# Kernel tuning notes

Hardware: AMD Instinct MI355X
Metric: run time of the kernel (lower is better)

Reference implementation:

```python
import jax, jax.numpy as jnp
import numpy as np


def setup_inputs() -> dict:
    key = jax.random.key(0)
    k1, k2, k3 = jax.random.split(key, 3)
    B, C, H, W = 4, 256, 96, 128
    F = 9
    return {
        "input1": jax.random.normal(k1, (B, C, H, W), dtype=jnp.float32),
        "input2": jax.random.normal(k2, (B, C, H, W), dtype=jnp.float32),
        "weights": jax.random.normal(k3, (C, F, F), dtype=jnp.float32),
        "filter_size": 9,
        "dilation": 2,
        "num_groups": 4,
    }


def _weighted_corr(input1, input2, weights, filter_size, dilation, num_groups):
    B, C, H, W = input1.shape
    F = filter_size
    G = num_groups
    Cg = C // G
    r = F // 2
    pad = r * dilation
    # zero-pad input2 spatially so out-of-bounds displacements contribute 0
    p2 = jnp.pad(input2, ((0, 0), (0, 0), (pad, pad), (pad, pad)))
    in1g = input1.reshape(B, G, Cg, H, W)
    outs = []  # one [B, G, H, W] map per window offset (dy, dx)
    for dy in range(F):
        for dx in range(F):
            shifted = p2[:, :, dy * dilation:dy * dilation + H,
                         dx * dilation:dx * dilation + W].reshape(B, G, Cg, H, W)
            wg = weights[:, dy, dx].reshape(G, Cg)
            outs.append(jnp.einsum('bgchw,bgchw,gc->bghw', in1g, shifted, wg))
    out = jnp.stack(outs, axis=2)  # [B, G, F*F, H, W]
    return out.reshape(B, G * F * F, H, W)


def reference(input1, input2, weights, filter_size, dilation, num_groups):
    return _weighted_corr(input1, input2, weights, filter_size, dilation, num_groups)
```

## Files before the change

### kernel.cpp

```cpp
#include <hip/hip_runtime.h>

#define B_   4
#define C_   256
#define H_   96
#define W_   128
#define F_   9
#define G_   4
#define CG   64
#define NC8  8
#define NO   81
#define HW_  (H_ * W_)

#define NDY   3
#define TROWS 8
#define TCOLS 80
#define PTE   (TROWS * TCOLS)
#define PNK   3

typedef _Float16 half2v __attribute__((ext_vector_type(2)));
typedef unsigned u32x4 __attribute__((ext_vector_type(4)));

__device__ __forceinline__ half2v u2h(unsigned u) {
    half2v h; __builtin_memcpy(&h, &u, 4); return h;
}
__device__ __forceinline__ unsigned h2u(half2v h) {
    unsigned u; __builtin_memcpy(&u, &h, 4); return u;
}
__device__ __forceinline__ half2v pkrtz(float a, float b) {
    auto r = __builtin_amdgcn_cvt_pkrtz(a, b);
    half2v h; __builtin_memcpy(&h, &r, 4); return h;
}
__device__ __forceinline__ unsigned pkrtz_u(float a, float b) {
    auto r = __builtin_amdgcn_cvt_pkrtz(a, b);
    unsigned u; __builtin_memcpy(&u, &r, 4); return u;
}

#if __has_builtin(__builtin_amdgcn_fdot2)
#define FDOT2(a, b, c) __builtin_amdgcn_fdot2((a), (b), (c), false)
#else
__device__ __forceinline__ float fdot2_fb(half2v a, half2v b, float c) {
    return c + (float)a[0] * (float)b[0] + (float)a[1] * (float)b[1];
}
#define FDOT2(a, b, c) fdot2_fb((a), (b), (c))
#endif

__global__ void pack_weights_kernel(const float* __restrict__ w,
                                    u32x4* __restrict__ wp) {
    int i = blockIdx.x * blockDim.x + threadIdx.x;
    if (i >= G_ * NC8 * NO) return;
    int o  = i % NO;
    int c8 = (i / NO) % NC8;
    int g  = i / (NO * NC8);
    const float* base = w + (size_t)(g * CG + 8 * c8) * NO + o;
    u32x4 r;
    r.x = pkrtz_u(base[0 * NO], base[1 * NO]);
    r.y = pkrtz_u(base[2 * NO], base[3 * NO]);
    r.z = pkrtz_u(base[4 * NO], base[5 * NO]);
    r.w = pkrtz_u(base[6 * NO], base[7 * NO]);
    wp[i] = r;
}

template <bool PACKED>
__global__ __launch_bounds__(256)
void wcorr_kernel(const float* __restrict__ in1, const float* __restrict__ in2,
                  const u32x4* __restrict__ wp, const float* __restrict__ wraw,
                  float* __restrict__ out) {
    __shared__ u32x4 tile[2][PTE];

    int bid  = blockIdx.x;
    int xcd  = bid & 7;
    int slot = bid >> 3;
    int pair = xcd + 8 * (slot / 144);
    int rem  = slot % 144;
    int pass = rem / 48;
    int sub  = rem % 48;
    int hblk = sub >> 1;
    int half = sub & 1;
    int b = pair >> 2, g = pair & 3;
    int h0 = hblk * 4;
    int w0 = half * 64;

    int t = threadIdx.x;
    int r = t >> 6;
    int x = t & 63;

    const float* in1g = in1 + (size_t)(b * C_ + g * CG) * HW_;
    const float* in2g = in2 + (size_t)(b * C_ + g * CG) * HW_;

    const int gr0 = h0 - 8 + 6 * pass;
    const int gc0 = w0 - 8;
    int po[PNK]; unsigned msk[PNK];
#pragma unroll
    for (int k = 0; k < PNK; ++k) {
        int pidx = k * 256 + t;
        int row  = pidx / TCOLS;
        int col  = pidx - row * TCOLS;
        int gr = gr0 + row, gc = gc0 + col;
        bool inb = (pidx < PTE) && gr >= 0 && gr < H_ && gc >= 0 && gc < W_;
        int off = gr * W_ + gc;
        off = off < 0 ? 0 : (off > HW_ - 1 ? HW_ - 1 : off);
        po[k]  = off;
        float m = inb ? 1.f : 0.f;
        msk[k] = pkrtz_u(m, m);
    }

    float acc[NDY * F_];
#pragma unroll
    for (int o = 0; o < NDY * F_; ++o) acc[o] = 0.f;

    float sv[PNK][8];

    auto LOADS = [&](int c8n) {
        const float* chb = in2g + (size_t)(8 * c8n) * HW_;
#pragma unroll
        for (int k = 0; k < PNK; ++k) {
            const float* q = chb + po[k];
#pragma unroll
            for (int j = 0; j < 8; ++j) sv[k][j] = q[(size_t)j * HW_];
        }
    };
    auto WRITE = [&](u32x4* dst) {
#pragma unroll
        for (int k = 0; k < PNK; ++k) {
            if (k < PNK - 1 || t < PTE - (PNK - 1) * 256) {
                half2v m = u2h(msk[k]);
                u32x4 e;
                e.x = h2u(u2h(pkrtz_u(sv[k][0], sv[k][1])) * m);
                e.y = h2u(u2h(pkrtz_u(sv[k][2], sv[k][3])) * m);
                e.z = h2u(u2h(pkrtz_u(sv[k][4], sv[k][5])) * m);
                e.w = h2u(u2h(pkrtz_u(sv[k][6], sv[k][7])) * m);
                dst[k * 256 + t] = e;
            }
        }
    };

    LOADS(0);
    WRITE(tile[0]);
    LOADS(1);

    const int in1off = (h0 + r) * W_ + (w0 + x);
    float a[8];
#pragma unroll
    for (int j = 0; j < 8; ++j) a[j] = in1g[in1off + (size_t)j * HW_];

    for (int c8 = 0; c8 < NC8; ++c8) {
        __syncthreads();

        if (c8 + 1 < NC8) WRITE(tile[(c8 + 1) & 1]);
        if (c8 + 2 < NC8) LOADS(c8 + 2);

        half2v ha0 = pkrtz(a[0], a[1]), ha1 = pkrtz(a[2], a[3]);
        half2v ha2 = pkrtz(a[4], a[5]), ha3 = pkrtz(a[6], a[7]);
        if (c8 + 1 < NC8) {
            const float* pp = in1g + (size_t)(8 * (c8 + 1)) * HW_ + in1off;
#pragma unroll
            for (int j = 0; j < 8; ++j) a[j] = pp[(size_t)j * HW_];
        }

        const u32x4* lt = tile[c8 & 1];
        const u32x4* wrow = PACKED ? (wp + ((size_t)g * NC8 + c8) * NO + pass * NDY * F_) : nullptr;
        const float* wr = wraw + (size_t)(g * CG + 8 * c8) * NO + pass * NDY * F_;

#pragma unroll
        for (int dyp = 0; dyp < NDY; ++dyp) {
            const u32x4* rowp = lt + (r + 2 * dyp) * TCOLS + x;
#pragma unroll
            for (int dx = 0; dx < F_; ++dx) {
                const int oo = dyp * F_ + dx;
                u32x4 uv = rowp[2 * dx];
                half2v w0h, w1h, w2h, w3h;
                if (PACKED) {
                    u32x4 wv = wrow[oo];
                    w0h = u2h(wv.x); w1h = u2h(wv.y);
                    w2h = u2h(wv.z); w3h = u2h(wv.w);
                } else {
                    w0h = pkrtz(wr[oo + 0 * NO], wr[oo + 1 * NO]);
                    w1h = pkrtz(wr[oo + 2 * NO], wr[oo + 3 * NO]);
                    w2h = pkrtz(wr[oo + 4 * NO], wr[oo + 5 * NO]);
                    w3h = pkrtz(wr[oo + 6 * NO], wr[oo + 7 * NO]);
                }
                float s = acc[oo];
                s = FDOT2(w0h * ha0, u2h(uv.x), s);
                s = FDOT2(w1h * ha1, u2h(uv.y), s);
                s = FDOT2(w2h * ha2, u2h(uv.z), s);
                s = FDOT2(w3h * ha3, u2h(uv.w), s);
                acc[oo] = s;
            }
        }
    }

    size_t obase = (((size_t)pair * NO + pass * NDY * F_) * H_ + (h0 + r)) * W_ + (w0 + x);
#pragma unroll
    for (int oo = 0; oo < NDY * F_; ++oo)
        out[obase + (size_t)oo * HW_] = acc[oo];
}

extern "C" void kernel_launch(void* const* d_in, const int* in_sizes, int n_in,
                              void* d_out, int out_size, void* d_ws, size_t ws_size,
                              hipStream_t stream) {
    const float* in1  = (const float*)d_in[0];
    const float* in2  = (const float*)d_in[1];
    const float* wraw = (const float*)d_in[2];
    float* out = (float*)d_out;

    const size_t wp_bytes = (size_t)G_ * NC8 * NO * 16;
    const int nblocks = 16 * 144;

    if (ws_size >= wp_bytes) {
        u32x4* wp = (u32x4*)d_ws;
        int n = G_ * NC8 * NO;
        pack_weights_kernel<<<(n + 255) / 256, 256, 0, stream>>>(wraw, wp);
        wcorr_kernel<true><<<nblocks, 256, 0, stream>>>(in1, in2, wp, wraw, out);
    } else {
        wcorr_kernel<false><<<nblocks, 256, 0, stream>>>(in1, in2, nullptr, wraw, out);
    }
}
```

Measured before the change: 74.60 us.

## Tile per single dy row with two outputs per thread sharing LDS reads

Each block now covers one dy and four full-width output rows, and each thread computes two output columns two apart. Because dilation is 2, both columns can share 10 LDS reads where 18 were needed before. The LDS tile is split by column parity with an XOR swizzle to avoid bank conflicts. in1 loads are now done per iteration with no prefetch, so their global latency is exposed, and the accumulator/grid shape changes (3456 blocks, 18 accumulators per thread).

```diff
diff --git a/kernel.cpp b/kernel.cpp
--- a/kernel.cpp
+++ b/kernel.cpp
@@ -11,10 +11,10 @@
 #define NO   81
 #define HW_  (H_ * W_)
 
-#define NDY   3
-#define TROWS 8
-#define TCOLS 80
-#define PTE   (TROWS * TCOLS)
+#define OROWS 4
+#define TCOLS 144
+#define PCOLS 72
+#define NENT  (OROWS * 2 * PCOLS)
 #define PNK   3
 
 typedef _Float16 half2v __attribute__((ext_vector_type(2)));
@@ -43,6 +43,10 @@
 }
 #define FDOT2(a, b, c) fdot2_fb((a), (b), (c))
 #endif
+
+__device__ __forceinline__ int swz(int col2) {
+    return col2 ^ ((col2 >> 3) & 7);
+}
 
 __global__ void pack_weights_kernel(const float* __restrict__ w,
                                     u32x4* __restrict__ wp) {
@@ -65,48 +69,54 @@
 void wcorr_kernel(const float* __restrict__ in1, const float* __restrict__ in2,
                   const u32x4* __restrict__ wp, const float* __restrict__ wraw,
                   float* __restrict__ out) {
-    __shared__ u32x4 tile[2][PTE];
-
-    int bid  = blockIdx.x;
-    int xcd  = bid & 7;
-    int slot = bid >> 3;
-    int pair = xcd + 8 * (slot / 144);
-    int rem  = slot % 144;
-    int pass = rem / 48;
-    int sub  = rem % 48;
-    int hblk = sub >> 1;
-    int half = sub & 1;
+    __shared__ u32x4 tile[2][NENT];
+
+    int bid   = blockIdx.x;
+    int xcd   = bid & 7;
+    int slot  = bid >> 3;
+    int tuple = slot / 9;
+    int dy    = slot - tuple * 9;
+    int T     = tuple * 8 + xcd;
+    int pair  = T & 15;
+    int hblk  = T >> 4;
     int b = pair >> 2, g = pair & 3;
-    int h0 = hblk * 4;
-    int w0 = half * 64;
-
-    int t = threadIdx.x;
-    int r = t >> 6;
-    int x = t & 63;
+    int h0 = hblk * OROWS;
+
+    int t   = threadIdx.x;
+    int row = t >> 6;
+    int i   = t & 63;
+    int j   = i >> 1;
+    int p   = i & 1;
+    const int c0 = 4 * j + p;
 
     const float* in1g = in1 + (size_t)(b * C_ + g * CG) * HW_;
     const float* in2g = in2 + (size_t)(b * C_ + g * CG) * HW_;
 
-    const int gr0 = h0 - 8 + 6 * pass;
-    const int gc0 = w0 - 8;
-    int po[PNK]; unsigned msk[PNK];
+    const int gr0 = h0 + 2 * dy - 8;
+    int po[PNK]; unsigned msk[PNK]; int lix[PNK];
 #pragma unroll
     for (int k = 0; k < PNK; ++k) {
         int pidx = k * 256 + t;
-        int row  = pidx / TCOLS;
-        int col  = pidx - row * TCOLS;
-        int gr = gr0 + row, gc = gc0 + col;
-        bool inb = (pidx < PTE) && gr >= 0 && gr < H_ && gc >= 0 && gc < W_;
+        int srow = pidx / TCOLS;
+        int col  = pidx - srow * TCOLS;
+        int gr = gr0 + srow, gc = col - 8;
+        bool inb = (pidx < NENT) && gr >= 0 && gr < H_ && gc >= 0 && gc < W_;
         int off = gr * W_ + gc;
         off = off < 0 ? 0 : (off > HW_ - 1 ? HW_ - 1 : off);
         po[k]  = off;
         float m = inb ? 1.f : 0.f;
         msk[k] = pkrtz_u(m, m);
-    }
-
-    float acc[NDY * F_];
-#pragma unroll
-    for (int o = 0; o < NDY * F_; ++o) acc[o] = 0.f;
+        lix[k] = (srow * 2 + (col & 1)) * PCOLS + swz(col >> 1);
+    }
+
+    int widx[10];
+#pragma unroll
+    for (int m = 0; m < 10; ++m)
+        widx[m] = (row * 2 + p) * PCOLS + swz(2 * j + m);
+
+    float acc0[F_], acc1[F_];
+#pragma unroll
+    for (int dx = 0; dx < F_; ++dx) { acc0[dx] = 0.f; acc1[dx] = 0.f; }
 
     float sv[PNK][8];
 
@@ -114,22 +124,24 @@
         const float* chb = in2g + (size_t)(8 * c8n) * HW_;
 #pragma unroll
         for (int k = 0; k < PNK; ++k) {
-            const float* q = chb + po[k];
-#pragma unroll
-            for (int j = 0; j < 8; ++j) sv[k][j] = q[(size_t)j * HW_];
+            if (k < PNK - 1 || t < NENT - (PNK - 1) * 256) {
+                const float* q = chb + po[k];
+#pragma unroll
+                for (int c = 0; c < 8; ++c) sv[k][c] = q[(size_t)c * HW_];
+            }
         }
     };
     auto WRITE = [&](u32x4* dst) {
 #pragma unroll
         for (int k = 0; k < PNK; ++k) {
-            if (k < PNK - 1 || t < PTE - (PNK - 1) * 256) {
+            if (k < PNK - 1 || t < NENT - (PNK - 1) * 256) {
                 half2v m = u2h(msk[k]);
                 u32x4 e;
                 e.x = h2u(u2h(pkrtz_u(sv[k][0], sv[k][1])) * m);
                 e.y = h2u(u2h(pkrtz_u(sv[k][2], sv[k][3])) * m);
                 e.z = h2u(u2h(pkrtz_u(sv[k][4], sv[k][5])) * m);
                 e.w = h2u(u2h(pkrtz_u(sv[k][6], sv[k][7])) * m);
-                dst[k * 256 + t] = e;
+                dst[lix[k]] = e;
             }
         }
     };
@@ -138,10 +150,7 @@
     WRITE(tile[0]);
     LOADS(1);
 
-    const int in1off = (h0 + r) * W_ + (w0 + x);
-    float a[8];
-#pragma unroll
-    for (int j = 0; j < 8; ++j) a[j] = in1g[in1off + (size_t)j * HW_];
+    const int in1off = (h0 + row) * W_ + c0;
 
     for (int c8 = 0; c8 < NC8; ++c8) {
         __syncthreads();
@@ -149,50 +158,72 @@
         if (c8 + 1 < NC8) WRITE(tile[(c8 + 1) & 1]);
         if (c8 + 2 < NC8) LOADS(c8 + 2);
 
-        half2v ha0 = pkrtz(a[0], a[1]), ha1 = pkrtz(a[2], a[3]);
-        half2v ha2 = pkrtz(a[4], a[5]), ha3 = pkrtz(a[6], a[7]);
-        if (c8 + 1 < NC8) {
-            const float* pp = in1g + (size_t)(8 * (c8 + 1)) * HW_ + in1off;
-#pragma unroll
-            for (int j = 0; j < 8; ++j) a[j] = pp[(size_t)j * HW_];
+        const float* ib = in1g + (size_t)(8 * c8) * HW_ + in1off;
+        half2v ha0, ha1, ha2, ha3, hb0, hb1, hb2, hb3;
+        {
+            float x0 = ib[0], x1 = ib[HW_], x2 = ib[2 * HW_], x3 = ib[3 * HW_];
+            float x4 = ib[4 * HW_], x5 = ib[5 * HW_], x6 = ib[6 * HW_], x7 = ib[7 * HW_];
+            ha0 = pkrtz(x0, x1); ha1 = pkrtz(x2, x3);
+            ha2 = pkrtz(x4, x5); ha3 = pkrtz(x6, x7);
+            float y0 = ib[2], y1 = ib[HW_ + 2], y2 = ib[2 * HW_ + 2], y3 = ib[3 * HW_ + 2];
+            float y4 = ib[4 * HW_ + 2], y5 = ib[5 * HW_ + 2], y6 = ib[6 * HW_ + 2], y7 = ib[7 * HW_ + 2];
+            hb0 = pkrtz(y0, y1); hb1 = pkrtz(y2, y3);
+            hb2 = pkrtz(y4, y5); hb3 = pkrtz(y6, y7);
         }
 
         const u32x4* lt = tile[c8 & 1];
-        const u32x4* wrow = PACKED ? (wp + ((size_t)g * NC8 + c8) * NO + pass * NDY * F_) : nullptr;
-        const float* wr = wraw + (size_t)(g * CG + 8 * c8) * NO + pass * NDY * F_;
-
-#pragma unroll
-        for (int dyp = 0; dyp < NDY; ++dyp) {
-            const u32x4* rowp = lt + (r + 2 * dyp) * TCOLS + x;
-#pragma unroll
-            for (int dx = 0; dx < F_; ++dx) {
-                const int oo = dyp * F_ + dx;
-                u32x4 uv = rowp[2 * dx];
+        const u32x4* wrow = PACKED ? (wp + ((size_t)g * NC8 + c8) * NO + dy * F_) : nullptr;
+        const float* wr = wraw + (size_t)(g * CG + 8 * c8) * NO + dy * F_;
+
+#pragma unroll
+        for (int m = 0; m < 10; ++m) {
+            u32x4 uv = lt[widx[m]];
+            if (m <= 8) {
                 half2v w0h, w1h, w2h, w3h;
                 if (PACKED) {
-                    u32x4 wv = wrow[oo];
-                    w0h = u2h(wv.x); w1h = u2h(wv.y);
-                    w2h = u2h(wv.z); w3h = u2h(wv.w);
+                    u32x4 wv = wrow[m];
+                    w0h = u2h(wv.x); w1h = u2h(wv.y); w2h = u2h(wv.z); w3h = u2h(wv.w);
                 } else {
-                    w0h = pkrtz(wr[oo + 0 * NO], wr[oo + 1 * NO]);
-                    w1h = pkrtz(wr[oo + 2 * NO], wr[oo + 3 * NO]);
-                    w2h = pkrtz(wr[oo + 4 * NO], wr[oo + 5 * NO]);
-                    w3h = pkrtz(wr[oo + 6 * NO], wr[oo + 7 * NO]);
+                    w0h = pkrtz(wr[m + 0 * NO], wr[m + 1 * NO]);
+                    w1h = pkrtz(wr[m + 2 * NO], wr[m + 3 * NO]);
+                    w2h = pkrtz(wr[m + 4 * NO], wr[m + 5 * NO]);
+                    w3h = pkrtz(wr[m + 6 * NO], wr[m + 7 * NO]);
                 }
-                float s = acc[oo];
+                float s = acc0[m];
                 s = FDOT2(w0h * ha0, u2h(uv.x), s);
                 s = FDOT2(w1h * ha1, u2h(uv.y), s);
                 s = FDOT2(w2h * ha2, u2h(uv.z), s);
                 s = FDOT2(w3h * ha3, u2h(uv.w), s);
-                acc[oo] = s;
-            }
-        }
-    }
-
-    size_t obase = (((size_t)pair * NO + pass * NDY * F_) * H_ + (h0 + r)) * W_ + (w0 + x);
-#pragma unroll
-    for (int oo = 0; oo < NDY * F_; ++oo)
-        out[obase + (size_t)oo * HW_] = acc[oo];
+                acc0[m] = s;
+            }
+            if (m >= 1) {
+                const int dx = m - 1;
+                half2v w0h, w1h, w2h, w3h;
+                if (PACKED) {
+                    u32x4 wv = wrow[dx];
+                    w0h = u2h(wv.x); w1h = u2h(wv.y); w2h = u2h(wv.z); w3h = u2h(wv.w);
+                } else {
+                    w0h = pkrtz(wr[dx + 0 * NO], wr[dx + 1 * NO]);
+                    w1h = pkrtz(wr[dx + 2 * NO], wr[dx + 3 * NO]);
+                    w2h = pkrtz(wr[dx + 4 * NO], wr[dx + 5 * NO]);
+                    w3h = pkrtz(wr[dx + 6 * NO], wr[dx + 7 * NO]);
+                }
+                float s = acc1[dx];
+                s = FDOT2(w0h * hb0, u2h(uv.x), s);
+                s = FDOT2(w1h * hb1, u2h(uv.y), s);
+                s = FDOT2(w2h * hb2, u2h(uv.z), s);
+                s = FDOT2(w3h * hb3, u2h(uv.w), s);
+                acc1[dx] = s;
+            }
+        }
+    }
+
+    size_t obase = (((size_t)(pair * NO + dy * F_)) * H_ + (h0 + row)) * W_ + c0;
+#pragma unroll
+    for (int dx = 0; dx < F_; ++dx) {
+        out[obase + (size_t)dx * HW_]     = acc0[dx];
+        out[obase + (size_t)dx * HW_ + 2] = acc1[dx];
+    }
 }
 
 extern "C" void kernel_launch(void* const* d_in, const int* in_sizes, int n_in,
@@ -204,7 +235,7 @@
     float* out = (float*)d_out;
 
     const size_t wp_bytes = (size_t)G_ * NC8 * NO * 16;
-    const int nblocks = 16 * 144;
+    const int nblocks = 8 * 48 * F_;
 
     if (ws_size >= wp_bytes) {
         u32x4* wp = (u32x4*)d_ws;
```

Result: slower. 91.21 us (+22.3%).

## Give each wave a private shared tile slice to drop block barriers

Applied to the files above, without the earlier changes.

Restructures the shared-memory staging so each wavefront (output row) loads and stores only the three input rows it reads itself, in its own double-buffered slice. This removes the per-channel-chunk __syncthreads. Global loads of input2 become paired 2-float vector loads with per-element masks. The cost is loading overlapping rows redundantly across waves (3 rows per wave instead of 8 shared rows per block) and relying on intra-wave ordering of LDS writes and reads without a barrier.

```diff
diff --git a/kernel.cpp b/kernel.cpp
--- a/kernel.cpp
+++ b/kernel.cpp
@@ -12,13 +12,14 @@
 #define HW_  (H_ * W_)
 
 #define NDY   3
-#define TROWS 8
+#define OROWS 4
 #define TCOLS 80
-#define PTE   (TROWS * TCOLS)
-#define PNK   3
+#define WENT  (NDY * TCOLS)
+#define NPRC  (NDY * 40)
 
 typedef _Float16 half2v __attribute__((ext_vector_type(2)));
 typedef unsigned u32x4 __attribute__((ext_vector_type(4)));
+typedef float    f32x2 __attribute__((ext_vector_type(2)));
 
 __device__ __forceinline__ half2v u2h(unsigned u) {
     half2v h; __builtin_memcpy(&h, &u, 4); return h;
@@ -65,7 +66,7 @@
 void wcorr_kernel(const float* __restrict__ in1, const float* __restrict__ in2,
                   const u32x4* __restrict__ wp, const float* __restrict__ wraw,
                   float* __restrict__ out) {
-    __shared__ u32x4 tile[2][PTE];
+    __shared__ u32x4 tile[OROWS * 2 * WENT];
 
     int bid  = blockIdx.x;
     int xcd  = bid & 7;
@@ -77,7 +78,7 @@
     int hblk = sub >> 1;
     int half = sub & 1;
     int b = pair >> 2, g = pair & 3;
-    int h0 = hblk * 4;
+    int h0 = hblk * OROWS;
     int w0 = half * 64;
 
     int t = threadIdx.x;
@@ -89,53 +90,64 @@
 
     const int gr0 = h0 - 8 + 6 * pass;
     const int gc0 = w0 - 8;
-    int po[PNK]; unsigned msk[PNK];
-#pragma unroll
-    for (int k = 0; k < PNK; ++k) {
-        int pidx = k * 256 + t;
-        int row  = pidx / TCOLS;
-        int col  = pidx - row * TCOLS;
-        int gr = gr0 + row, gc = gc0 + col;
-        bool inb = (pidx < PTE) && gr >= 0 && gr < H_ && gc >= 0 && gc < W_;
+    int po[2]; unsigned mA[2], mB[2]; int lix[2];
+#pragma unroll
+    for (int k = 0; k < 2; ++k) {
+        int pi = k * 64 + x;
+        int pl = pi / 40;
+        int pc = pi - 40 * pl;
+        int gr = gr0 + r + 2 * pl;
+        int gc = gc0 + 2 * pc;
+        bool grv = (pi < NPRC) && gr >= 0 && gr < H_;
+        float f0 = (grv && gc >= 0 && gc < W_) ? 1.f : 0.f;
+        float f1 = (grv && gc + 1 >= 0 && gc + 1 < W_) ? 1.f : 0.f;
         int off = gr * W_ + gc;
-        off = off < 0 ? 0 : (off > HW_ - 1 ? HW_ - 1 : off);
-        po[k]  = off;
-        float m = inb ? 1.f : 0.f;
-        msk[k] = pkrtz_u(m, m);
+        off = off < 0 ? 0 : (off > HW_ - 2 ? HW_ - 2 : off);
+        po[k] = off;
+        mA[k] = pkrtz_u(f0, f0);
+        mB[k] = pkrtz_u(f1, f1);
+        lix[k] = pl * TCOLS + 2 * pc;
     }
 
     float acc[NDY * F_];
 #pragma unroll
     for (int o = 0; o < NDY * F_; ++o) acc[o] = 0.f;
 
-    float sv[PNK][8];
+    f32x2 sv[2][8];
 
     auto LOADS = [&](int c8n) {
         const float* chb = in2g + (size_t)(8 * c8n) * HW_;
 #pragma unroll
-        for (int k = 0; k < PNK; ++k) {
+        for (int k = 0; k < 2; ++k) {
             const float* q = chb + po[k];
 #pragma unroll
-            for (int j = 0; j < 8; ++j) sv[k][j] = q[(size_t)j * HW_];
+            for (int j = 0; j < 8; ++j)
+                sv[k][j] = *(const f32x2*)(q + (size_t)j * HW_);
         }
     };
-    auto WRITE = [&](u32x4* dst) {
-#pragma unroll
-        for (int k = 0; k < PNK; ++k) {
-            if (k < PNK - 1 || t < PTE - (PNK - 1) * 256) {
-                half2v m = u2h(msk[k]);
-                u32x4 e;
-                e.x = h2u(u2h(pkrtz_u(sv[k][0], sv[k][1])) * m);
-                e.y = h2u(u2h(pkrtz_u(sv[k][2], sv[k][3])) * m);
-                e.z = h2u(u2h(pkrtz_u(sv[k][4], sv[k][5])) * m);
-                e.w = h2u(u2h(pkrtz_u(sv[k][6], sv[k][7])) * m);
-                dst[k * 256 + t] = e;
+    auto WRITE = [&](int buf) {
+        u32x4* wt = tile + (r * 2 + buf) * WENT;
+#pragma unroll
+        for (int k = 0; k < 2; ++k) {
+            if (k == 0 || x < NPRC - 64) {
+                half2v m0 = u2h(mA[k]), m1 = u2h(mB[k]);
+                u32x4 e0, e1;
+                e0.x = h2u(u2h(pkrtz_u(sv[k][0].x, sv[k][1].x)) * m0);
+                e0.y = h2u(u2h(pkrtz_u(sv[k][2].x, sv[k][3].x)) * m0);
+                e0.z = h2u(u2h(pkrtz_u(sv[k][4].x, sv[k][5].x)) * m0);
+                e0.w = h2u(u2h(pkrtz_u(sv[k][6].x, sv[k][7].x)) * m0);
+                e1.x = h2u(u2h(pkrtz_u(sv[k][0].y, sv[k][1].y)) * m1);
+                e1.y = h2u(u2h(pkrtz_u(sv[k][2].y, sv[k][3].y)) * m1);
+                e1.z = h2u(u2h(pkrtz_u(sv[k][4].y, sv[k][5].y)) * m1);
+                e1.w = h2u(u2h(pkrtz_u(sv[k][6].y, sv[k][7].y)) * m1);
+                wt[lix[k]]     = e0;
+                wt[lix[k] + 1] = e1;
             }
         }
     };
 
     LOADS(0);
-    WRITE(tile[0]);
+    WRITE(0);
     LOADS(1);
 
     const int in1off = (h0 + r) * W_ + (w0 + x);
@@ -144,30 +156,27 @@
     for (int j = 0; j < 8; ++j) a[j] = in1g[in1off + (size_t)j * HW_];
 
     for (int c8 = 0; c8 < NC8; ++c8) {
-        __syncthreads();
-
-        if (c8 + 1 < NC8) WRITE(tile[(c8 + 1) & 1]);
+        if (c8 + 1 < NC8) WRITE((c8 + 1) & 1);
         if (c8 + 2 < NC8) LOADS(c8 + 2);
 
         half2v ha0 = pkrtz(a[0], a[1]), ha1 = pkrtz(a[2], a[3]);
         half2v ha2 = pkrtz(a[4], a[5]), ha3 = pkrtz(a[6], a[7]);
         if (c8 + 1 < NC8) {
-            const float* pp = in1g + (size_t)(8 * (c8 + 1)) * HW_ + in1off;
-#pragma unroll
-            for (int j = 0; j < 8; ++j) a[j] = pp[(size_t)j * HW_];
-        }
-
-        const u32x4* lt = tile[c8 & 1];
+            const float* ib = in1g + (size_t)(8 * (c8 + 1)) * HW_ + in1off;
+#pragma unroll
+            for (int j = 0; j < 8; ++j) a[j] = ib[(size_t)j * HW_];
+        }
+
+        const u32x4* lb = tile + (r * 2 + (c8 & 1)) * WENT + x;
         const u32x4* wrow = PACKED ? (wp + ((size_t)g * NC8 + c8) * NO + pass * NDY * F_) : nullptr;
         const float* wr = wraw + (size_t)(g * CG + 8 * c8) * NO + pass * NDY * F_;
 
 #pragma unroll
         for (int dyp = 0; dyp < NDY; ++dyp) {
-            const u32x4* rowp = lt + (r + 2 * dyp) * TCOLS + x;
 #pragma unroll
             for (int dx = 0; dx < F_; ++dx) {
                 const int oo = dyp * F_ + dx;
-                u32x4 uv = rowp[2 * dx];
+                u32x4 uv = lb[dyp * TCOLS + 2 * dx];
                 half2v w0h, w1h, w2h, w3h;
                 if (PACKED) {
                     u32x4 wv = wrow[oo];
@@ -204,7 +213,7 @@
     float* out = (float*)d_out;
 
     const size_t wp_bytes = (size_t)G_ * NC8 * NO * 16;
-    const int nblocks = 16 * 144;
+    const int nblocks = 16 * 3 * 24 * 2;
 
     if (ws_size >= wp_bytes) {
         u32x4* wp = (u32x4*)d_ws;
```

Measured after the change: 77.63 us. 4.1% more time.
